# Optimization experiments

Measured on AMD Instinct MI355X. Metric: run time of the kernel, lower is better.

Reference implementation:

```python
import jax, jax.numpy as jnp
import numpy as np
from jax import lax

T, I, H, L = 4096, 101, 1000, 4  # seq len, letters_num, hidden, num_layers


def setup_inputs() -> dict:
    key = jax.random.key(0)
    ks = jax.random.split(key, 9)
    s = 0.03  # weight scale ~ 1/sqrt(H)
    return {
        "x": jax.random.normal(ks[0], (T, 1, I), jnp.float32),
        "enc_Wih": jax.random.normal(ks[1], (L, 4 * H, I), jnp.float32) * s,
        "enc_Whh": jax.random.normal(ks[2], (L, 4 * H, H), jnp.float32) * s,
        "enc_bih": jax.random.normal(ks[3], (L, 4 * H), jnp.float32) * s,
        "enc_bhh": jax.random.normal(ks[4], (L, 4 * H), jnp.float32) * s,
        "dec_Wih": jax.random.normal(ks[5], (L, 4 * I, H), jnp.float32) * s,
        "dec_Whh": jax.random.normal(ks[6], (L, 4 * I, I), jnp.float32) * s,
        "dec_bih": jax.random.normal(ks[7], (L, 4 * I), jnp.float32) * s,
        "dec_bhh": jax.random.normal(ks[8], (L, 4 * I), jnp.float32) * s,
        "length": T,
    }


def _lstm_cell(x, h, c, Wih, Whh, bih, bhh):
    # PyTorch LSTMCell gate order: i, f, g, o
    gates = x @ Wih.T + bih + h @ Whh.T + bhh  # [T, 4*Hout]
    i, f, g, o = jnp.split(gates, 4, axis=-1)
    c = jax.nn.sigmoid(f) * c + jax.nn.sigmoid(i) * jnp.tanh(g)
    h = jax.nn.sigmoid(o) * jnp.tanh(c)
    return h, c


def _stack(xt, Wih, Whh, bih, bhh, hout):
    # Hidden is reset per timestep in the original, so timesteps are a batch;
    # only the layer chain is sequential. Every layer consumes the same xt.
    t = xt.shape[0]
    init = (jnp.zeros((t, hout), xt.dtype), jnp.zeros((t, hout), xt.dtype))

    def body(carry, p):
        h, c = carry
        wih, whh, bi, bh = p
        h, c = _lstm_cell(xt, h, c, wih, whh, bi, bh)
        return (h, c), None

    (h, _), _ = lax.scan(body, init, (Wih, Whh, bih, bhh))
    return h


def reference(x, enc_Wih, enc_Whh, enc_bih, enc_bhh,
              dec_Wih, dec_Whh, dec_bih, dec_bhh, length):
    xt = x[:, 0, :]                      # [T, I]
    hdim = enc_Whh.shape[-1]
    odim = dec_Whh.shape[-1]
    enc = jax.nn.relu(_stack(xt, enc_Wih, enc_Whh, enc_bih, enc_bhh, hdim))  # [T, H]
    dec = _stack(enc, dec_Wih, dec_Whh, dec_bih, dec_bhh, odim)              # [T, O]
    out = jax.nn.log_softmax(dec, axis=-1)[:, None, :]                       # [T, 1, O]
    return out
```

## Files before the change

### kernel.cpp

```cpp
#include <hip/hip_runtime.h>
#include <cstdint>
#include <cstddef>
#include <cmath>

typedef __bf16 bf16_t;
typedef __bf16 bf16x8 __attribute__((ext_vector_type(8)));
typedef float floatx4 __attribute__((ext_vector_type(4)));

#define AS1 __attribute__((address_space(1)))
#define AS3 __attribute__((address_space(3)))

__device__ __forceinline__ void gload_lds16(const bf16_t* g, bf16_t* l) {
    __builtin_amdgcn_global_load_lds((AS1 void*)(uintptr_t)(g), (AS3 void*)(l), 16, 0, 0);
}

__device__ __forceinline__ float sigf(float x) { return 1.0f / (1.0f + __expf(-x)); }
__device__ __forceinline__ float tanhfast(float x) { return 1.0f - 2.0f / (__expf(2.0f * x) + 1.0f); }

template<int BM>
__global__ __launch_bounds__(256, 4)
void gemm_lstm(const bf16_t* __restrict__ A, const bf16_t* __restrict__ B,
               const float* __restrict__ bias,
               float* __restrict__ zout, int ldZ,
               float* __restrict__ c, int EP,
               bf16_t* __restrict__ hb, int ldH, int hoff,
               int K, int ldA, int ldB, int relu, int czero)
{
    constexpr int AI = BM / 32;
    __shared__ bf16_t As[BM * 64];
    __shared__ bf16_t Bs[128 * 64];
    const int tid  = threadIdx.x;
    const int lane = tid & 63;
    const int w    = tid >> 6;
    const int wm   = (w & 1) * (BM / 2);
    const int wn   = (w >> 1) * 64;
    const int m0   = blockIdx.y * BM;
    const int n0   = blockIdx.x * 128;

    floatx4 zero = {0.0f, 0.0f, 0.0f, 0.0f};
    floatx4 acc[AI][4];
#pragma unroll
    for (int i = 0; i < AI; ++i)
#pragma unroll
        for (int j = 0; j < 4; ++j) acc[i][j] = zero;

    const int srow = lane >> 3;
    const int sk   = ((lane & 7) ^ srow) * 8;
    const int fr   = lane & 15;
    const int fx   = fr & 7;

    const bf16_t* Ag = A + (size_t)(m0 + srow) * ldA + sk;
    const bf16_t* Bg = B + (size_t)(n0 + srow) * ldB + sk;

    for (int k0 = 0; k0 < K; k0 += 64) {
        __syncthreads();
#pragma unroll
        for (int j = 0; j < AI; ++j) {
            int r0 = (w * AI + j) * 8;
            gload_lds16(Ag + (size_t)r0 * ldA + k0, As + r0 * 64 + lane * 8);
        }
#pragma unroll
        for (int j = 0; j < 4; ++j) {
            int r0 = (w * 4 + j) * 8;
            gload_lds16(Bg + (size_t)r0 * ldB + k0, Bs + r0 * 64 + lane * 8);
        }
        __syncthreads();
#pragma unroll
        for (int kk = 0; kk < 64; kk += 32) {
            const int pc = ((((kk >> 3) + (lane >> 4)) ^ fx) << 3);
            bf16x8 af[AI], bfr[4];
#pragma unroll
            for (int i = 0; i < AI; ++i)
                af[i] = *(const bf16x8*)(As + (wm + i * 16 + fr) * 64 + pc);
#pragma unroll
            for (int j = 0; j < 4; ++j)
                bfr[j] = *(const bf16x8*)(Bs + (wn + j * 16 + fr) * 64 + pc);
#pragma unroll
            for (int i = 0; i < AI; ++i)
#pragma unroll
                for (int j = 0; j < 4; ++j)
                    acc[i][j] = __builtin_amdgcn_mfma_f32_16x16x32_bf16(af[i], bfr[j], acc[i][j], 0, 0, 0);
        }
    }

    const int crow = (lane >> 4) * 4;
    const int ccol = lane & 15;
    const int nn   = n0 + wn;
    float bi[4];
#pragma unroll
    for (int j = 0; j < 4; ++j) bi[j] = bias[nn + j * 16 + ccol];

    if (zout) {
#pragma unroll
        for (int i = 0; i < AI; ++i) {
#pragma unroll
            for (int r = 0; r < 4; ++r) {
                int t = m0 + wm + i * 16 + crow + r;
                float* zr = zout + (size_t)t * ldZ + nn + ccol;
#pragma unroll
                for (int j = 0; j < 4; ++j) zr[j * 16] = acc[i][j][r] + bi[j];
            }
        }
        return;
    }

    const int e = (nn >> 2) + ccol;
#pragma unroll
    for (int i = 0; i < AI; ++i) {
#pragma unroll
        for (int r = 0; r < 4; ++r) {
            int t = m0 + wm + i * 16 + crow + r;
            float g0 = acc[i][0][r] + bi[0];
            float g1 = acc[i][1][r] + bi[1];
            float g2 = acc[i][2][r] + bi[2];
            float g3 = acc[i][3][r] + bi[3];
            size_t cix = (size_t)t * EP + e;
            float cold = 0.0f;
            if (!czero) cold = c[cix];
            float cv = sigf(g1) * cold + sigf(g0) * tanhfast(g2);
            c[cix] = cv;
            float hv = sigf(g3) * tanhfast(cv);
            if (relu) hv = fmaxf(hv, 0.0f);
            hb[(size_t)t * ldH + hoff + e] = (bf16_t)hv;
        }
    }
}

__global__ __launch_bounds__(256)
void dec_fused(const float* __restrict__ Z, const bf16_t* __restrict__ Wd,
               float* __restrict__ out)
{
    __shared__ bf16_t hB[16 * 136];
    __shared__ float  hS[16 * 132];
    const int tid  = threadIdx.x;
    const int lane = tid & 63;
    const int w    = tid >> 6;
    const int m0   = blockIdx.x * 16;
    const int ccol = lane & 15;
    const int crow = (lane >> 4) * 4;
    const int ksl  = (lane >> 4) * 8;

    float cst[2][4];
    floatx4 zerov = {0.0f, 0.0f, 0.0f, 0.0f};

    for (int l = 0; l < 4; ++l) {
        floatx4 acc[2][4];
#pragma unroll
        for (int q = 0; q < 2; ++q)
#pragma unroll
            for (int g = 0; g < 4; ++g) acc[q][g] = zerov;

        if (l > 0) {
#pragma unroll
            for (int kk = 0; kk < 128; kk += 32) {
                bf16x8 a = *(const bf16x8*)(hB + ccol * 136 + kk + ksl);
#pragma unroll
                for (int j = 0; j < 8; ++j) {
                    const bf16_t* wp = Wd + (size_t)(l * 512 + w * 128 + j * 16 + ccol) * 1152
                                          + 1024 + kk + ksl;
                    bf16x8 b = *(const bf16x8*)wp;
                    acc[j >> 2][j & 3] =
                        __builtin_amdgcn_mfma_f32_16x16x32_bf16(a, b, acc[j >> 2][j & 3], 0, 0, 0);
                }
            }
        }
        __syncthreads();

#pragma unroll
        for (int q = 0; q < 2; ++q) {
#pragma unroll
            for (int r = 0; r < 4; ++r) {
                int t = m0 + crow + r;
                const float* zr = Z + (size_t)t * 2048 + l * 512 + w * 128 + q * 64 + ccol;
                float g0 = acc[q][0][r] + zr[0];
                float g1 = acc[q][1][r] + zr[16];
                float g2 = acc[q][2][r] + zr[32];
                float g3 = acc[q][3][r] + zr[48];
                float cold = (l == 0) ? 0.0f : cst[q][r];
                float cv = sigf(g1) * cold + sigf(g0) * tanhfast(g2);
                cst[q][r] = cv;
                float hv = sigf(g3) * tanhfast(cv);
                int e = w * 32 + q * 16 + ccol;
                if (l < 3) hB[(crow + r) * 136 + e] = (bf16_t)hv;
                else       hS[(crow + r) * 132 + e] = hv;
            }
        }
        __syncthreads();
    }

#pragma unroll
    for (int rr = 0; rr < 4; ++rr) {
        int row = w * 4 + rr;
        const float* hr = hS + row * 132;
        float v1 = (lane < 101)      ? hr[lane]      : -INFINITY;
        float v2 = (lane + 64 < 101) ? hr[lane + 64] : -INFINITY;
        float m = fmaxf(v1, v2);
#pragma unroll
        for (int off = 32; off > 0; off >>= 1) m = fmaxf(m, __shfl_down(m, off));
        m = __shfl(m, 0);
        float ev = ((lane < 101) ? __expf(v1 - m) : 0.0f)
                 + ((lane + 64 < 101) ? __expf(v2 - m) : 0.0f);
#pragma unroll
        for (int off = 32; off > 0; off >>= 1) ev += __shfl_down(ev, off);
        float lse = m + __logf(__shfl(ev, 0));
        float* orow = out + (size_t)(m0 + row) * 101;
        if (lane < 101)      orow[lane]      = v1 - lse;
        if (lane + 64 < 101) orow[lane + 64] = v2 - lse;
    }
}

__global__ void pack_all(const float* __restrict__ x,
                         const float* __restrict__ eWih, const float* __restrict__ eWhh,
                         const float* __restrict__ ebih, const float* __restrict__ ebhh,
                         const float* __restrict__ dWih, const float* __restrict__ dWhh,
                         const float* __restrict__ dbih, const float* __restrict__ dbhh,
                         bf16_t* __restrict__ Aenc, bf16_t* __restrict__ Wenc,
                         bf16_t* __restrict__ Wdec,
                         float* __restrict__ bse, float* __restrict__ bsd)
{
    const int b = blockIdx.x;
    if (b < 9216) {
        int gid = b * 256 + threadIdx.x;
        int row = gid / 144, grp = gid - row * 144;
        int l = row >> 12, p = row & 4095;
        int g = (p >> 4) & 3, e = ((p >> 6) << 4) + (p & 15);
        int c0 = grp * 8;
        float v[8];
#pragma unroll
        for (int u = 0; u < 8; ++u) v[u] = 0.0f;
        if (e < 1000) {
            size_t r = (size_t)l * 4000 + g * 1000 + e;
            if (c0 >= 128 && c0 < 1128) {
                const float* src = eWhh + r * 1000 + (c0 - 128);
                float4 a = *(const float4*)src;
                float4 bq = *(const float4*)(src + 4);
                v[0]=a.x; v[1]=a.y; v[2]=a.z; v[3]=a.w; v[4]=bq.x; v[5]=bq.y; v[6]=bq.z; v[7]=bq.w;
            } else if (c0 < 128) {
                const float* src = eWih + r * 101;
#pragma unroll
                for (int u = 0; u < 8; ++u) { int cc = c0 + u; if (cc < 101) v[u] = src[cc]; }
            }
        }
        bf16x8 o;
#pragma unroll
        for (int u = 0; u < 8; ++u) o[u] = (bf16_t)v[u];
        *(bf16x8*)(Wenc + (size_t)row * 1152 + c0) = o;
    } else if (b < 11520) {
        int gid = (b - 9216) * 256 + threadIdx.x;
        int row = gid / 144, grp = gid - row * 144;
        int c0  = grp * 8;
        float v[8];
#pragma unroll
        for (int u = 0; u < 8; ++u) v[u] = 0.0f;
        if (c0 < 101) {
            const float* src = x + (size_t)row * 101;
#pragma unroll
            for (int u = 0; u < 8; ++u) { int cc = c0 + u; if (cc < 101) v[u] = src[cc]; }
        }
        bf16x8 o;
#pragma unroll
        for (int u = 0; u < 8; ++u) o[u] = (bf16_t)v[u];
        *(bf16x8*)(Aenc + (size_t)row * 1152 + c0) = o;
    } else if (b < 12672) {
        int gid = (b - 11520) * 256 + threadIdx.x;
        int row = gid / 144, grp = gid - row * 144;
        int l = row >> 9, p = row & 511;
        int g = (p >> 4) & 3, e = ((p >> 6) << 4) + (p & 15);
        int c0 = grp * 8;
        float v[8];
#pragma unroll
        for (int u = 0; u < 8; ++u) v[u] = 0.0f;
        if (e < 101) {
            size_t r = (size_t)l * 404 + g * 101 + e;
            if (c0 < 1000) {
                const float* src = dWih + r * 1000 + c0;
                float4 a = *(const float4*)src;
                float4 bq = *(const float4*)(src + 4);
                v[0]=a.x; v[1]=a.y; v[2]=a.z; v[3]=a.w; v[4]=bq.x; v[5]=bq.y; v[6]=bq.z; v[7]=bq.w;
            } else if (c0 >= 1024 && c0 < 1128) {
                const float* src = dWhh + r * 101;
#pragma unroll
                for (int u = 0; u < 8; ++u) { int cc = c0 + u; if (cc < 1125) v[u] = src[cc - 1024]; }
            }
        }
        bf16x8 o;
#pragma unroll
        for (int u = 0; u < 8; ++u) o[u] = (bf16_t)v[u];
        *(bf16x8*)(Wdec + (size_t)row * 1152 + c0) = o;
    } else {
        int idx = (b - 12672) * 256 + threadIdx.x;
        if (idx < 16384) {
            int l = idx >> 12, p = idx & 4095;
            int g = (p >> 4) & 3, e = ((p >> 6) << 4) + (p & 15);
            bse[idx] = (e < 1000) ? (ebih[l * 4000 + g * 1000 + e] + ebhh[l * 4000 + g * 1000 + e]) : 0.0f;
        } else {
            int k = idx - 16384;
            int l = k >> 9, p = k & 511;
            int g = (p >> 4) & 3, e = ((p >> 6) << 4) + (p & 15);
            bsd[k] = (e < 101) ? (dbih[l * 404 + g * 101 + e] + dbhh[l * 404 + g * 101 + e]) : 0.0f;
        }
    }
}

extern "C" void kernel_launch(void* const* d_in, const int* in_sizes, int n_in,
                              void* d_out, int out_size, void* d_ws, size_t ws_size,
                              hipStream_t stream)
{
    (void)in_sizes; (void)n_in; (void)out_size; (void)ws_size;
    const float* x    = (const float*)d_in[0];
    const float* eWih = (const float*)d_in[1];
    const float* eWhh = (const float*)d_in[2];
    const float* ebih = (const float*)d_in[3];
    const float* ebhh = (const float*)d_in[4];
    const float* dWih = (const float*)d_in[5];
    const float* dWhh = (const float*)d_in[6];
    const float* dbih = (const float*)d_in[7];
    const float* dbhh = (const float*)d_in[8];

    char* ws = (char*)d_ws;
    bf16_t* Aenc = (bf16_t*)(ws);
    bf16_t* Wenc = (bf16_t*)(ws + 9437184);
    bf16_t* Adec = (bf16_t*)(ws + 47185920);
    bf16_t* Wdec = (bf16_t*)(ws + 56623104);
    float*  bse  = (float*) (ws + 61341696);
    float*  bsd  = (float*) (ws + 61407232);
    float*  cenc = (float*) (ws + 61415424);
    float*  Z    = (float*)(ws + 9437184);

    pack_all<<<12744, 256, 0, stream>>>(x, eWih, eWhh, ebih, ebhh, dWih, dWhh, dbih, dbhh,
                                        Aenc, Wenc, Wdec, bse, bsd);

    for (int l = 0; l < 4; ++l) {
        gemm_lstm<128><<<dim3(32, 32), 256, 0, stream>>>(
            Aenc, Wenc + (size_t)l * 4096 * 1152, bse + l * 4096,
            nullptr, 0,
            cenc, 1024,
            (l < 3) ? Aenc : Adec, 1152, (l < 3) ? 128 : 0,
            (l == 0) ? 128 : 1152, 1152, 1152, (l == 3) ? 1 : 0, (l == 0) ? 1 : 0);
    }

    gemm_lstm<128><<<dim3(16, 32), 256, 0, stream>>>(
        Adec, Wdec, bsd,
        Z, 2048,
        nullptr, 0,
        nullptr, 0, 0,
        1024, 1152, 1152, 0, 0);

    dec_fused<<<256, 256, 0, stream>>>(Z, Wdec, (float*)d_out);
}
```

Baseline: 342.8 us.

## Fuse decoder input projection GEMM into decoder LSTM recurrence kernel

Removes the separate GEMM that wrote decoder input-gate preactivations to a large fp32 buffer. The new decoder kernel stages each 32-row slice of encoder output in LDS and computes all four layers' input projections into registers before running the layer chain. This eliminates a kernel launch and the Z write/read traffic, at the cost of fewer blocks (128), heavy accumulator register use, and weights read directly from global memory per wave.

```diff
diff --git a/kernel.cpp b/kernel.cpp
--- a/kernel.cpp
+++ b/kernel.cpp
@@ -21,7 +21,6 @@
 __global__ __launch_bounds__(256, 4)
 void gemm_lstm(const bf16_t* __restrict__ A, const bf16_t* __restrict__ B,
                const float* __restrict__ bias,
-               float* __restrict__ zout, int ldZ,
                float* __restrict__ c, int EP,
                bf16_t* __restrict__ hb, int ldH, int hoff,
                int K, int ldA, int ldB, int relu, int czero)
@@ -90,20 +89,6 @@
 #pragma unroll
     for (int j = 0; j < 4; ++j) bi[j] = bias[nn + j * 16 + ccol];
 
-    if (zout) {
-#pragma unroll
-        for (int i = 0; i < AI; ++i) {
-#pragma unroll
-            for (int r = 0; r < 4; ++r) {
-                int t = m0 + wm + i * 16 + crow + r;
-                float* zr = zout + (size_t)t * ldZ + nn + ccol;
-#pragma unroll
-                for (int j = 0; j < 4; ++j) zr[j * 16] = acc[i][j][r] + bi[j];
-            }
-        }
-        return;
-    }
-
     const int e = (nn >> 2) + ccol;
 #pragma unroll
     for (int i = 0; i < AI; ++i) {
@@ -126,65 +111,98 @@
     }
 }
 
-__global__ __launch_bounds__(256)
-void dec_fused(const float* __restrict__ Z, const bf16_t* __restrict__ Wd,
-               float* __restrict__ out)
+__global__ __launch_bounds__(512, 2)
+void dec_fused2(const bf16_t* __restrict__ Adec, const bf16_t* __restrict__ Wd,
+                const float* __restrict__ bsd, float* __restrict__ out)
 {
-    __shared__ bf16_t hB[16 * 136];
-    __shared__ float  hS[16 * 132];
+    __shared__ bf16_t hA[32 * 1032];
+    __shared__ bf16_t hB[32 * 136];
+    __shared__ float  hS[32 * 132];
     const int tid  = threadIdx.x;
     const int lane = tid & 63;
     const int w    = tid >> 6;
-    const int m0   = blockIdx.x * 16;
-    const int ccol = lane & 15;
+    const int m0   = blockIdx.x * 32;
+    const int fr   = lane & 15;
+    const int ksl  = (lane >> 4) * 8;
     const int crow = (lane >> 4) * 4;
-    const int ksl  = (lane >> 4) * 8;
+
+    for (int u = tid; u < 4096; u += 512) {
+        int r = u >> 7, c8 = u & 127;
+        *(bf16x8*)(hA + r * 1032 + c8 * 8) =
+            *(const bf16x8*)(Adec + (size_t)(m0 + r) * 1152 + c8 * 8);
+    }
+    __syncthreads();
+
+    floatx4 zerov = {0.0f, 0.0f, 0.0f, 0.0f};
+    floatx4 acc[2][4][4];
+#pragma unroll
+    for (int i = 0; i < 2; ++i)
+#pragma unroll
+        for (int l = 0; l < 4; ++l)
+#pragma unroll
+            for (int j = 0; j < 4; ++j) acc[i][l][j] = zerov;
+
+#pragma unroll 4
+    for (int kk = 0; kk < 32; ++kk) {
+        bf16x8 a0 = *(const bf16x8*)(hA + fr * 1032 + kk * 32 + ksl);
+        bf16x8 a1 = *(const bf16x8*)(hA + (16 + fr) * 1032 + kk * 32 + ksl);
+#pragma unroll
+        for (int l = 0; l < 4; ++l)
+#pragma unroll
+            for (int j = 0; j < 4; ++j) {
+                bf16x8 b = *(const bf16x8*)(Wd +
+                    (size_t)(l * 512 + w * 64 + j * 16 + fr) * 1152 + kk * 32 + ksl);
+                acc[0][l][j] = __builtin_amdgcn_mfma_f32_16x16x32_bf16(a0, b, acc[0][l][j], 0, 0, 0);
+                acc[1][l][j] = __builtin_amdgcn_mfma_f32_16x16x32_bf16(a1, b, acc[1][l][j], 0, 0, 0);
+            }
+    }
+
+#pragma unroll
+    for (int l = 0; l < 4; ++l)
+#pragma unroll
+        for (int j = 0; j < 4; ++j) {
+            float bi = bsd[l * 512 + w * 64 + j * 16 + fr];
+            acc[0][l][j] += bi;
+            acc[1][l][j] += bi;
+        }
 
     float cst[2][4];
-    floatx4 zerov = {0.0f, 0.0f, 0.0f, 0.0f};
-
     for (int l = 0; l < 4; ++l) {
-        floatx4 acc[2][4];
-#pragma unroll
-        for (int q = 0; q < 2; ++q)
-#pragma unroll
-            for (int g = 0; g < 4; ++g) acc[q][g] = zerov;
-
         if (l > 0) {
-#pragma unroll
-            for (int kk = 0; kk < 128; kk += 32) {
-                bf16x8 a = *(const bf16x8*)(hB + ccol * 136 + kk + ksl);
-#pragma unroll
-                for (int j = 0; j < 8; ++j) {
-                    const bf16_t* wp = Wd + (size_t)(l * 512 + w * 128 + j * 16 + ccol) * 1152
-                                          + 1024 + kk + ksl;
-                    bf16x8 b = *(const bf16x8*)wp;
-                    acc[j >> 2][j & 3] =
-                        __builtin_amdgcn_mfma_f32_16x16x32_bf16(a, b, acc[j >> 2][j & 3], 0, 0, 0);
+            bf16x8 a2[4][2];
+#pragma unroll
+            for (int kk = 0; kk < 4; ++kk) {
+                a2[kk][0] = *(const bf16x8*)(hB + fr * 136 + kk * 32 + ksl);
+                a2[kk][1] = *(const bf16x8*)(hB + (16 + fr) * 136 + kk * 32 + ksl);
+            }
+#pragma unroll
+            for (int kk = 0; kk < 4; ++kk)
+#pragma unroll
+                for (int j = 0; j < 4; ++j) {
+                    bf16x8 b = *(const bf16x8*)(Wd +
+                        (size_t)(l * 512 + w * 64 + j * 16 + fr) * 1152 + 1024 + kk * 32 + ksl);
+                    acc[0][l][j] = __builtin_amdgcn_mfma_f32_16x16x32_bf16(a2[kk][0], b, acc[0][l][j], 0, 0, 0);
+                    acc[1][l][j] = __builtin_amdgcn_mfma_f32_16x16x32_bf16(a2[kk][1], b, acc[1][l][j], 0, 0, 0);
                 }
-            }
-        }
-        __syncthreads();
-
-#pragma unroll
-        for (int q = 0; q < 2; ++q) {
+            __syncthreads();
+        }
+#pragma unroll
+        for (int i = 0; i < 2; ++i)
 #pragma unroll
             for (int r = 0; r < 4; ++r) {
-                int t = m0 + crow + r;
-                const float* zr = Z + (size_t)t * 2048 + l * 512 + w * 128 + q * 64 + ccol;
-                float g0 = acc[q][0][r] + zr[0];
-                float g1 = acc[q][1][r] + zr[16];
-                float g2 = acc[q][2][r] + zr[32];
-                float g3 = acc[q][3][r] + zr[48];
-                float cold = (l == 0) ? 0.0f : cst[q][r];
+                float g0 = acc[i][l][0][r];
+                float g1 = acc[i][l][1][r];
+                float g2 = acc[i][l][2][r];
+                float g3 = acc[i][l][3][r];
+                float cold = (l == 0) ? 0.0f : cst[i][r];
                 float cv = sigf(g1) * cold + sigf(g0) * tanhfast(g2);
-                cst[q][r] = cv;
+                cst[i][r] = cv;
                 float hv = sigf(g3) * tanhfast(cv);
-                int e = w * 32 + q * 16 + ccol;
-                if (l < 3) hB[(crow + r) * 136 + e] = (bf16_t)hv;
-                else       hS[(crow + r) * 132 + e] = hv;
-            }
-        }
+                int row = i * 16 + crow + r;
+                int e   = w * 16 + fr;
+                if (l < 3) hB[row * 136 + e] = (bf16_t)hv;
+                else       hS[row * 132 + e] = hv;
+            }
         __syncthreads();
     }
 
@@ -325,7 +343,6 @@
     float*  bse  = (float*) (ws + 61341696);
     float*  bsd  = (float*) (ws + 61407232);
     float*  cenc = (float*) (ws + 61415424);
-    float*  Z    = (float*)(ws + 9437184);
 
     pack_all<<<12744, 256, 0, stream>>>(x, eWih, eWhh, ebih, ebhh, dWih, dWhh, dbih, dbhh,
                                         Aenc, Wenc, Wdec, bse, bsd);
@@ -333,18 +350,10 @@
     for (int l = 0; l < 4; ++l) {
         gemm_lstm<128><<<dim3(32, 32), 256, 0, stream>>>(
             Aenc, Wenc + (size_t)l * 4096 * 1152, bse + l * 4096,
-            nullptr, 0,
             cenc, 1024,
             (l < 3) ? Aenc : Adec, 1152, (l < 3) ? 128 : 0,
             (l == 0) ? 128 : 1152, 1152, 1152, (l == 3) ? 1 : 0, (l == 0) ? 1 : 0);
     }
 
-    gemm_lstm<128><<<dim3(16, 32), 256, 0, stream>>>(
-        Adec, Wdec, bsd,
-        Z, 2048,
-        nullptr, 0,
-        nullptr, 0, 0,
-        1024, 1152, 1152, 0, 0);
-
-    dec_fused<<<256, 256, 0, stream>>>(Z, Wdec, (float*)d_out);
-}
+    dec_fused2<<<128, 512, 0, stream>>>(Adec, Wdec, bsd, (float*)d_out);
+}
```

New measurement: 440.5 us. 28.5% more time.

## Interleave decoder gate pre-activations and widen decoder block to 512 threads

Applied to the files above, without the earlier changes.

The Z output of the decoder input GEMM is now stored gate-interleaved as float4 per (row, layer, unit), so each thread writes one 16-byte value instead of four scattered scalars. The fused decoder kernel reads those float4s directly and runs with 8 waves instead of 4, each wave handling 16 units and a single accumulator set. This is meant to cut scattered global traffic and shorten the per-wave serial recurrent work. The cost is more threads per block, which may lower the number of resident blocks per CU.

```diff
diff --git a/kernel.cpp b/kernel.cpp
--- a/kernel.cpp
+++ b/kernel.cpp
@@ -17,11 +17,11 @@
 __device__ __forceinline__ float sigf(float x) { return 1.0f / (1.0f + __expf(-x)); }
 __device__ __forceinline__ float tanhfast(float x) { return 1.0f - 2.0f / (__expf(2.0f * x) + 1.0f); }
 
-template<int BM>
+template<int BM, int MODE>
 __global__ __launch_bounds__(256, 4)
 void gemm_lstm(const bf16_t* __restrict__ A, const bf16_t* __restrict__ B,
                const float* __restrict__ bias,
-               float* __restrict__ zout, int ldZ,
+               float* __restrict__ zout,
                float* __restrict__ c, int EP,
                bf16_t* __restrict__ hb, int ldH, int hoff,
                int K, int ldA, int ldB, int relu, int czero)
@@ -90,15 +90,20 @@
 #pragma unroll
     for (int j = 0; j < 4; ++j) bi[j] = bias[nn + j * 16 + ccol];
 
-    if (zout) {
+    if constexpr (MODE == 1) {
+        const int lz = nn >> 9;
+        const int ez = ((nn & 511) >> 6) * 16 + ccol;
 #pragma unroll
         for (int i = 0; i < AI; ++i) {
 #pragma unroll
             for (int r = 0; r < 4; ++r) {
                 int t = m0 + wm + i * 16 + crow + r;
-                float* zr = zout + (size_t)t * ldZ + nn + ccol;
-#pragma unroll
-                for (int j = 0; j < 4; ++j) zr[j * 16] = acc[i][j][r] + bi[j];
+                float4 g4;
+                g4.x = acc[i][0][r] + bi[0];
+                g4.y = acc[i][1][r] + bi[1];
+                g4.z = acc[i][2][r] + bi[2];
+                g4.w = acc[i][3][r] + bi[3];
+                *(float4*)(zout + ((size_t)t * 512 + lz * 128 + ez) * 4) = g4;
             }
         }
         return;
@@ -126,9 +131,9 @@
     }
 }
 
-__global__ __launch_bounds__(256)
-void dec_fused(const float* __restrict__ Z, const bf16_t* __restrict__ Wd,
-               float* __restrict__ out)
+__global__ __launch_bounds__(512)
+void dec_fused3(const float* __restrict__ Zp, const bf16_t* __restrict__ Wd,
+                float* __restrict__ out)
 {
     __shared__ bf16_t hB[16 * 136];
     __shared__ float  hS[16 * 132];
@@ -136,61 +141,59 @@
     const int lane = tid & 63;
     const int w    = tid >> 6;
     const int m0   = blockIdx.x * 16;
-    const int ccol = lane & 15;
+    const int fr   = lane & 15;
+    const int ksl  = (lane >> 4) * 8;
     const int crow = (lane >> 4) * 4;
-    const int ksl  = (lane >> 4) * 8;
-
-    float cst[2][4];
+
+    float cst[4];
     floatx4 zerov = {0.0f, 0.0f, 0.0f, 0.0f};
 
     for (int l = 0; l < 4; ++l) {
-        floatx4 acc[2][4];
-#pragma unroll
-        for (int q = 0; q < 2; ++q)
-#pragma unroll
-            for (int g = 0; g < 4; ++g) acc[q][g] = zerov;
+        float4 z4[4];
+#pragma unroll
+        for (int r = 0; r < 4; ++r)
+            z4[r] = *(const float4*)(Zp +
+                ((size_t)(m0 + crow + r) * 512 + l * 128 + w * 16 + fr) * 4);
+
+        floatx4 acc[4];
+#pragma unroll
+        for (int j = 0; j < 4; ++j) acc[j] = zerov;
 
         if (l > 0) {
 #pragma unroll
-            for (int kk = 0; kk < 128; kk += 32) {
-                bf16x8 a = *(const bf16x8*)(hB + ccol * 136 + kk + ksl);
-#pragma unroll
-                for (int j = 0; j < 8; ++j) {
-                    const bf16_t* wp = Wd + (size_t)(l * 512 + w * 128 + j * 16 + ccol) * 1152
-                                          + 1024 + kk + ksl;
-                    bf16x8 b = *(const bf16x8*)wp;
-                    acc[j >> 2][j & 3] =
-                        __builtin_amdgcn_mfma_f32_16x16x32_bf16(a, b, acc[j >> 2][j & 3], 0, 0, 0);
+            for (int kk = 0; kk < 4; ++kk) {
+                bf16x8 a = *(const bf16x8*)(hB + fr * 136 + kk * 32 + ksl);
+#pragma unroll
+                for (int j = 0; j < 4; ++j) {
+                    bf16x8 b = *(const bf16x8*)(Wd +
+                        (size_t)(l * 512 + w * 64 + j * 16 + fr) * 1152 + 1024 + kk * 32 + ksl);
+                    acc[j] = __builtin_amdgcn_mfma_f32_16x16x32_bf16(a, b, acc[j], 0, 0, 0);
                 }
             }
         }
         __syncthreads();
 
 #pragma unroll
-        for (int q = 0; q < 2; ++q) {
-#pragma unroll
-            for (int r = 0; r < 4; ++r) {
-                int t = m0 + crow + r;
-                const float* zr = Z + (size_t)t * 2048 + l * 512 + w * 128 + q * 64 + ccol;
-                float g0 = acc[q][0][r] + zr[0];
-                float g1 = acc[q][1][r] + zr[16];
-                float g2 = acc[q][2][r] + zr[32];
-                float g3 = acc[q][3][r] + zr[48];
-                float cold = (l == 0) ? 0.0f : cst[q][r];
-                float cv = sigf(g1) * cold + sigf(g0) * tanhfast(g2);
-                cst[q][r] = cv;
-                float hv = sigf(g3) * tanhfast(cv);
-                int e = w * 32 + q * 16 + ccol;
-                if (l < 3) hB[(crow + r) * 136 + e] = (bf16_t)hv;
-                else       hS[(crow + r) * 132 + e] = hv;
-            }
+        for (int r = 0; r < 4; ++r) {
+            float g0 = acc[0][r] + z4[r].x;
+            float g1 = acc[1][r] + z4[r].y;
+            float g2 = acc[2][r] + z4[r].z;
+            float g3 = acc[3][r] + z4[r].w;
+            float cold = (l == 0) ? 0.0f : cst[r];
+            float cv = sigf(g1) * cold + sigf(g0) * tanhfast(g2);
+            cst[r] = cv;
+            float hv = sigf(g3) * tanhfast(cv);
+            int row = crow + r;
+            int e   = w * 16 + fr;
+            if (l < 3) hB[row * 136 + e] = (bf16_t)hv;
+            else       hS[row * 132 + e] = hv;
         }
         __syncthreads();
     }
 
 #pragma unroll
-    for (int rr = 0; rr < 4; ++rr) {
-        int row = w * 4 + rr;
+    for (int rr = 0; rr < 2; ++rr) {
+        int row = w * 2 + rr;
         const float* hr = hS + row * 132;
         float v1 = (lane < 101)      ? hr[lane]      : -INFINITY;
         float v2 = (lane + 64 < 101) ? hr[lane + 64] : -INFINITY;
@@ -325,26 +328,26 @@
     float*  bse  = (float*) (ws + 61341696);
     float*  bsd  = (float*) (ws + 61407232);
     float*  cenc = (float*) (ws + 61415424);
-    float*  Z    = (float*)(ws + 9437184);
+    float*  Zp   = (float*)(ws + 9437184);
 
     pack_all<<<12744, 256, 0, stream>>>(x, eWih, eWhh, ebih, ebhh, dWih, dWhh, dbih, dbhh,
                                         Aenc, Wenc, Wdec, bse, bsd);
 
     for (int l = 0; l < 4; ++l) {
-        gemm_lstm<128><<<dim3(32, 32), 256, 0, stream>>>(
+        gemm_lstm<128, 0><<<dim3(32, 32), 256, 0, stream>>>(
             Aenc, Wenc + (size_t)l * 4096 * 1152, bse + l * 4096,
-            nullptr, 0,
+            nullptr,
             cenc, 1024,
             (l < 3) ? Aenc : Adec, 1152, (l < 3) ? 128 : 0,
             (l == 0) ? 128 : 1152, 1152, 1152, (l == 3) ? 1 : 0, (l == 0) ? 1 : 0);
     }
 
-    gemm_lstm<128><<<dim3(16, 32), 256, 0, stream>>>(
+    gemm_lstm<128, 1><<<dim3(16, 32), 256, 0, stream>>>(
         Adec, Wdec, bsd,
-        Z, 2048,
+        Zp,
         nullptr, 0,
         nullptr, 0, 0,
         1024, 1152, 1152, 0, 0);
 
-    dec_fused<<<256, 256, 0, stream>>>(Z, Wdec, (float*)d_out);
-}
+    dec_fused3<<<256, 512, 0, stream>>>(Zp, Wdec, (float*)d_out);
+}
```

Result: faster. 324.9 us, median of 2 (-5.2%).
